# Optimization experiments

Measured on AMD Instinct MI355X. Metric: run time of the kernel, lower is better.

The kernel has to match this reference:

```python
import jax, jax.numpy as jnp
import numpy as np

T, D, H, E, V, WN = 4096, 128, 512, 256, 50000, 4


def setup_inputs() -> dict:
    key = jax.random.key(0)
    ks = jax.random.split(key, 16)
    x = jax.random.normal(ks[0], (T, D), jnp.float32)
    word_ids = jax.random.randint(ks[1], (T, WN), 0, V, dtype=jnp.int32)
    lens = jax.random.randint(ks[2], (T, WN), 2, 7)  # word lengths in [2,6]
    starts = jnp.arange(T)[:, None] - lens + 1       # word ending at t starts at t-len+1
    valid = starts >= 0
    word_mask = jnp.logical_and(valid, jax.random.uniform(ks[3], (T, WN)) < 0.3)
    word_starts = jnp.maximum(starts, 0).astype(jnp.int32)
    h0 = jax.random.normal(ks[4], (H,), jnp.float32)
    c0 = jax.random.normal(ks[5], (H,), jnp.float32)
    emb = jax.random.normal(ks[6], (V, E), jnp.float32)
    s_d, s_h, s_e = 1.0 / np.sqrt(D), 1.0 / np.sqrt(H), 1.0 / np.sqrt(E)
    W = jax.random.normal(ks[7], (D, 3 * H), jnp.float32) * s_d
    U = jax.random.normal(ks[8], (H, 3 * H), jnp.float32) * s_h
    b = jnp.zeros((3 * H,), jnp.float32)
    Wa = jax.random.normal(ks[9], (D, H), jnp.float32) * s_d
    Ua = jax.random.normal(ks[10], (H, H), jnp.float32) * s_h
    ba = jnp.zeros((H,), jnp.float32)
    Ww = jax.random.normal(ks[11], (E, 3 * H), jnp.float32) * s_e
    Uw = jax.random.normal(ks[12], (H, 3 * H), jnp.float32) * s_h
    bw = jnp.zeros((3 * H,), jnp.float32)
    return {"x": x, "word_ids": word_ids, "word_starts": word_starts,
            "word_mask": word_mask, "h0": h0, "c0": c0, "emb": emb,
            "W": W, "U": U, "b": b, "Wa": Wa, "Ua": Ua, "ba": ba,
            "Ww": Ww, "Uw": Uw, "bw": bw}


def _lattice_forward(x, word_ids, word_starts, word_mask, h0, c0, emb,
                     W, U, b, Wa, Ua, ba, Ww, Uw, bw):
    Tn = x.shape[0]
    Hn = h0.shape[0]

    def step(carry, inp):
        h_prev, c_prev, Hbuf, Cbuf, t = carry
        xt, wids, wstarts, wmask = inp
        # --- WordLSTMCell for lexicon words ending at t (started at wstarts) ---
        h_s = Hbuf[wstarts]                     # [WN, H] post-step states at starts
        c_s = Cbuf[wstarts]                     # [WN, H]
        x_w = emb[wids]                         # [WN, E] (word_dropout in eval mode)
        gw = x_w @ Ww + h_s @ Uw + bw           # [WN, 3H]
        f_w, i_w, g_w = jnp.split(gw, 3, axis=-1)
        c_w = jax.nn.sigmoid(f_w) * c_s + jax.nn.sigmoid(i_w) * jnp.tanh(g_w)
        # --- MultiInputLSTMCell at position t ---
        gates = xt @ W + h_prev @ U + b         # [3H]
        i_g, o_g, g_g = jnp.split(gates, 3)
        i_g = jax.nn.sigmoid(i_g)
        o_g = jax.nn.sigmoid(o_g)
        g_g = jnp.tanh(g_g)
        alpha = jax.nn.sigmoid(xt @ Wa + ba + c_w @ Ua)   # [WN, H]
        e = jnp.exp(jnp.concatenate([i_g[None, :], alpha], axis=0))  # [1+WN, H]
        m = jnp.concatenate([jnp.ones((1,), bool), wmask])
        e = e * m[:, None]
        wts = e / jnp.sum(e, axis=0)
        cand = jnp.concatenate([g_g[None, :], c_w], axis=0)
        c_soft = jnp.sum(wts * cand, axis=0)
        c_plain = (1.0 - i_g) * c_prev + i_g * g_g        # candidate_num == 0 branch
        c1 = jnp.where(jnp.any(wmask), c_soft, c_plain)
        h1 = o_g * jnp.tanh(c1)
        Hbuf = Hbuf.at[t].set(h1)
        Cbuf = Cbuf.at[t].set(c1)
        return (h1, c1, Hbuf, Cbuf, t + 1), (h1, c1)

    carry0 = (h0, c0, jnp.zeros((Tn, Hn), x.dtype), jnp.zeros((Tn, Hn), x.dtype),
              jnp.int32(0))
    _, (hs, cs) = jax.lax.scan(step, carry0, (x, word_ids, word_starts, word_mask))
    return jnp.concatenate([hs, cs], axis=-1)   # [T, 2H] hidden|cell states


def reference(x, word_ids, word_starts, word_mask, h0, c0, emb,
              W, U, b, Wa, Ua, ba, Ww, Uw, bw):
    return _lattice_forward(x, word_ids, word_starts, word_mask, h0, c0, emb,
                            W, U, b, Wa, Ua, ba, Ww, Uw, bw)
```

## Files before the change

### kernel.cpp

```cpp
#include <hip/hip_runtime.h>
#include <hip/hip_bf16.h>

typedef __hip_bfloat16 bf16;
typedef _Float16 half2v __attribute__((ext_vector_type(2)));

#define T_LEN 4096
#define D_IN  128
#define H_DIM 512
#define E_DIM 256
#define WNUM  4
#define G3    1536
#define NBLK  64

#define OFF_MODE   0ull
#define OFF_FMODE  4ull
#define OFF_HPK    16384ull
#define OFF_CWPK   (OFF_HPK + 8ull*512ull*4ull)
#define OFF_A      65536ull
#define OFF_AXA    (OFF_A   + 4096ull*1536ull*2ull)
#define OFF_GW0    (OFF_AXA + 4096ull*512ull*2ull)

__device__ __forceinline__ float bf2f(bf16 h) {
  unsigned short u = __builtin_bit_cast(unsigned short, h);
  unsigned int i = ((unsigned int)u) << 16;
  return __builtin_bit_cast(float, i);
}
__device__ __forceinline__ unsigned short f2bfbits(float f) {
  return __builtin_bit_cast(unsigned short, __float2bfloat16(f));
}
__device__ __forceinline__ unsigned int packbf(float a, float b) {
  return (unsigned int)f2bfbits(a) | ((unsigned int)f2bfbits(b) << 16);
}
__device__ __forceinline__ float sigm(float x) { return 1.f / (1.f + __expf(-x)); }
__device__ __forceinline__ float tanhfast(float x) { return 1.f - 2.f / (__expf(2.f * x) + 1.f); }

#if __has_builtin(__builtin_amdgcn_fdot2)
__device__ __forceinline__ float fdot2(half2v a, half2v b, float c) {
  return __builtin_amdgcn_fdot2(a, b, c, false);
}
#else
__device__ __forceinline__ float fdot2(half2v a, half2v b, float c) {
  return c + (float)a.x * (float)b.x + (float)a.y * (float)b.y;
}
#endif

__device__ __forceinline__ half2v make2(float a, float b) {
  half2v r; r.x = (_Float16)a; r.y = (_Float16)b; return r;
}

__device__ __forceinline__ unsigned int pack16(float v, int tag) {
  _Float16 h = (_Float16)v;
  unsigned short b = __builtin_bit_cast(unsigned short, h);
  return ((unsigned int)tag << 16) | (unsigned int)b;
}
__device__ __forceinline__ _Float16 unpack16(unsigned int v) {
  return __builtin_bit_cast(_Float16, (unsigned short)(v & 0xffffu));
}
__device__ __forceinline__ unsigned int aload(const unsigned int* p) {
  return __hip_atomic_load(p, __ATOMIC_RELAXED, __HIP_MEMORY_SCOPE_AGENT);
}
__device__ __forceinline__ void astore(unsigned int* p, unsigned int v) {
  __hip_atomic_store(p, v, __ATOMIC_RELAXED, __HIP_MEMORY_SCOPE_AGENT);
}

__device__ __forceinline__ float ldf(const void* p, size_t i, int fm) {
  return fm ? ((const float*)p)[i] : bf2f(((const bf16*)p)[i]);
}
__device__ __forceinline__ void ld8(const void* p, size_t i, int fm, float* o) {
  if (fm) {
    const float* q = (const float*)p + i;
    float4 a = *(const float4*)q, b2 = *(const float4*)(q + 4);
    o[0]=a.x; o[1]=a.y; o[2]=a.z; o[3]=a.w; o[4]=b2.x; o[5]=b2.y; o[6]=b2.z; o[7]=b2.w;
  } else {
    uint4 raw = *(const uint4*)((const bf16*)p + i);
    unsigned int u[4] = {raw.x, raw.y, raw.z, raw.w};
#pragma unroll
    for (int j = 0; j < 4; ++j) {
      o[2*j]   = __builtin_bit_cast(float, u[j] << 16);
      o[2*j+1] = __builtin_bit_cast(float, u[j] & 0xffff0000u);
    }
  }
}
__device__ __forceinline__ void ld4(const void* p, size_t i, int fm, float* o) {
  if (fm) {
    float4 a = *(const float4*)((const float*)p + i);
    o[0]=a.x; o[1]=a.y; o[2]=a.z; o[3]=a.w;
  } else {
    uint2 raw = *(const uint2*)((const bf16*)p + i);
    o[0] = __builtin_bit_cast(float, raw.x << 16);
    o[1] = __builtin_bit_cast(float, raw.x & 0xffff0000u);
    o[2] = __builtin_bit_cast(float, raw.y << 16);
    o[3] = __builtin_bit_cast(float, raw.y & 0xffff0000u);
  }
}
__device__ __forceinline__ bool readmask(const void* p, int idx, int mode) {
  switch (mode) {
    case 0:  return ((const int*)p)[idx] != 0;
    case 1:  return ((const unsigned char*)p)[idx] != 0;
    case 2:  return ((const unsigned short*)p)[idx] != 0;
    default: return ((const unsigned int*)p)[idx] != 0;
  }
}

__global__ void k_init(const void* __restrict__ mask_p, const void* __restrict__ h0_p,
                       unsigned char* __restrict__ ws) {
  int tid = threadIdx.x;
  __shared__ int s_b1, s_bf, s_f32, s_votes;
  if (tid == 0) { s_b1 = 0; s_bf = 0; s_f32 = 0; s_votes = 0; }
  __syncthreads();
  int b1 = 0, bfh = 0, f32h = 0;
  const unsigned int* dv = (const unsigned int*)mask_p;
  for (int i = tid; i < 4096; i += 256) {
    unsigned int d = dv[i];
    if (((d >> 8) & 0xFFu) == 1u || ((d >> 16) & 0xFFu) == 1u || ((d >> 24) & 0xFFu) == 1u) b1 = 1;
    if ((d & 0xFFFFu) == 0x3F80u) bfh = 1;
    if (d == 0x3F800000u) f32h = 1;
  }
  if (b1)  atomicOr(&s_b1, 1);
  if (bfh) atomicOr(&s_bf, 1);
  if (f32h) atomicOr(&s_f32, 1);
  if (tid < 128) {
    unsigned int d = ((const unsigned int*)h0_p)[tid];
    int e = (int)((d >> 23) & 0xFF);
    if (e >= 100 && e <= 140) atomicAdd(&s_votes, 1);
  }
  __syncthreads();
  if (tid == 0) {
    int mode = s_b1 ? 1 : (s_bf ? 2 : (s_f32 ? 3 : 0));
    *(int*)(ws + OFF_MODE)  = mode;
    *(int*)(ws + OFF_FMODE) = (s_votes >= 64) ? 1 : 0;
  }
}

__global__ __launch_bounds__(256) void k_xgemm(
    const void* __restrict__ x, const void* __restrict__ W, const void* __restrict__ b,
    const void* __restrict__ Wa, const void* __restrict__ ba, unsigned char* __restrict__ ws) {
  const int fm = *(const int*)(ws + OFF_FMODE);
  bf16* A   = (bf16*)(ws + OFF_A);
  bf16* Axa = (bf16*)(ws + OFF_AXA);
  const int tid = threadIdx.x;
  const int t0 = blockIdx.x * 8;
  __shared__ float sx[8][128];
  {
    int flat = tid * 4, r = flat >> 7, k = flat & 127;
    ld4(x, (size_t)(t0 + r) * D_IN + k, fm, &sx[r][k]);
  }
  __syncthreads();
  const bool isA = (tid < 192);
  const int c0 = isA ? tid * 8 : (tid - 192) * 8;
  const void* M = isA ? W : Wa;
  const int ldm = isA ? G3 : H_DIM;
  float acc[8][8];
#pragma unroll
  for (int r = 0; r < 8; ++r)
#pragma unroll
    for (int c = 0; c < 8; ++c) acc[r][c] = 0.f;
  for (int k = 0; k < D_IN; ++k) {
    float wv[8];
    ld8(M, (size_t)k * ldm + c0, fm, wv);
#pragma unroll
    for (int r = 0; r < 8; ++r) {
      float xv = sx[r][k];
#pragma unroll
      for (int c = 0; c < 8; ++c) acc[r][c] += xv * wv[c];
    }
  }
  float bias[8];
  ld8(isA ? b : ba, c0, fm, bias);
#pragma unroll
  for (int r = 0; r < 8; ++r) {
    uint4 o;
    o.x = packbf(acc[r][0] + bias[0], acc[r][1] + bias[1]);
    o.y = packbf(acc[r][2] + bias[2], acc[r][3] + bias[3]);
    o.z = packbf(acc[r][4] + bias[4], acc[r][5] + bias[5]);
    o.w = packbf(acc[r][6] + bias[6], acc[r][7] + bias[7]);
    if (isA) *(uint4*)(A + (size_t)(t0 + r) * G3 + c0) = o;
    else     *(uint4*)(Axa + (size_t)(t0 + r) * H_DIM + c0) = o;
  }
}

__global__ __launch_bounds__(256) void k_wgemm(
    const int* __restrict__ wids, const void* __restrict__ wmask,
    const void* __restrict__ emb, const void* __restrict__ Ww, const void* __restrict__ bw,
    unsigned char* __restrict__ ws) {
  const int mode = *(const int*)(ws + OFF_MODE);
  const int fm   = *(const int*)(ws + OFF_FMODE);
  bf16* GW0 = (bf16*)(ws + OFF_GW0);
  const int tid = threadIdx.x;
  const int r0 = blockIdx.x * 8;
  bool m[8]; bool any = false;
#pragma unroll
  for (int r = 0; r < 8; ++r) {
    bool mm = readmask(wmask, r0 + r, mode);
    m[r] = mm; any |= mm;
  }
  if (!any) return;
  __shared__ float se[8][E_DIM];
#pragma unroll
  for (int r = 0; r < 8; ++r)
    if (m[r]) {
      int wid = wids[r0 + r];
      se[r][tid] = ldf(emb, (size_t)wid * E_DIM + tid, fm);
    }
  __syncthreads();
  if (tid < 192) {
    const int c0 = tid * 8;
    float acc[8][8];
#pragma unroll
    for (int r = 0; r < 8; ++r)
#pragma unroll
      for (int c = 0; c < 8; ++c) acc[r][c] = 0.f;
    for (int k = 0; k < E_DIM; ++k) {
      float wv[8];
      ld8(Ww, (size_t)k * G3 + c0, fm, wv);
#pragma unroll
      for (int r = 0; r < 8; ++r)
        if (m[r]) {
          float xv = se[r][k];
#pragma unroll
          for (int c = 0; c < 8; ++c) acc[r][c] += xv * wv[c];
        }
    }
    float bias[8];
    ld8(bw, c0, fm, bias);
#pragma unroll
    for (int r = 0; r < 8; ++r)
      if (m[r]) {
        uint4 o;
        o.x = packbf(acc[r][0] + bias[0], acc[r][1] + bias[1]);
        o.y = packbf(acc[r][2] + bias[2], acc[r][3] + bias[3]);
        o.z = packbf(acc[r][4] + bias[4], acc[r][5] + bias[5]);
        o.w = packbf(acc[r][6] + bias[6], acc[r][7] + bias[7]);
        *(uint4*)(GW0 + (size_t)(r0 + r) * G3 + c0) = o;
      }
  }
}

#define PASS(slotptr, wt, accvar) do {                                  \
    float _acc = 0.f;                                                   \
    const _Float16* _vp = (slotptr) + 8 * rg;                           \
    _Pragma("unroll")                                                   \
    for (int _m = 0; _m < 8; ++_m) {                                    \
      float4 _raw = *(const float4*)(_vp + 64 * _m);                    \
      half2v _h0 = __builtin_bit_cast(half2v, _raw.x);                  \
      half2v _h1 = __builtin_bit_cast(half2v, _raw.y);                  \
      half2v _h2 = __builtin_bit_cast(half2v, _raw.z);                  \
      half2v _h3 = __builtin_bit_cast(half2v, _raw.w);                  \
      _acc = fdot2(_h0, wt[_m * 4 + 0], _acc);                          \
      _acc = fdot2(_h1, wt[_m * 4 + 1], _acc);                          \
      _acc = fdot2(_h2, wt[_m * 4 + 2], _acc);                          \
      _acc = fdot2(_h3, wt[_m * 4 + 3], _acc);                          \
    }                                                                   \
    accvar = _acc;                                                      \
  } while (0)

__global__ __launch_bounds__(256, 1) void k_seq(
    const int* __restrict__ wstarts, const void* __restrict__ wmask,
    const void* __restrict__ h0_p, const void* __restrict__ c0_p,
    const void* __restrict__ U, const void* __restrict__ Uw, const void* __restrict__ Ua,
    unsigned char* __restrict__ ws, void* __restrict__ outp) {
  const int tid = threadIdx.x;
  const int blk = blockIdx.x;
  const int wv = tid >> 6;
  const int lane = tid & 63;
  const int cg = lane >> 3;
  const int rg = lane & 7;
  const int kbase = blk * 8 + wv * 2;

  const int mode = *(const int*)(ws + OFF_MODE);
  const int fm   = *(const int*)(ws + OFF_FMODE);
  const bf16* A   = (const bf16*)(ws + OFF_A);
  const bf16* Axa = (const bf16*)(ws + OFF_AXA);
  const bf16* GW0 = (const bf16*)(ws + OFF_GW0);
  unsigned int* HPK  = (unsigned int*)(ws + OFF_HPK);
  unsigned int* CWPK = (unsigned int*)(ws + OFF_CWPK);

  __shared__ __align__(16) _Float16 hring[8][520];
  __shared__ __align__(16) _Float16 cwlds[WNUM][520];
  __shared__ float cring[8][8];
  __shared__ float scr[4][8];
  __shared__ float cwown[4][WNUM][2];

  {
    _Float16* hz = &hring[0][0];
    for (int i = tid; i < 8 * 520; i += 256) hz[i] = (_Float16)0.f;
    _Float16* cz = &cwlds[0][0];
    for (int i = tid; i < WNUM * 520; i += 256) cz[i] = (_Float16)0.f;
    if (tid < 64) (&cring[0][0])[tid] = 0.f;
    if (tid < 32) (&scr[0][0])[tid] = 0.f;
    if (tid < 32) (&cwown[0][0][0])[tid] = 0.f;
  }

  half2v wU[32], wUw[32], wUa[32];
  {
    const int gate = cg >> 1;
    const int klw = cg & 1;
    const int colU = gate * H_DIM + (kbase + klw);
    const int colA = kbase + cg;
#pragma unroll
    for (int mq = 0; mq < 32; ++mq) {
      int mm = mq >> 2, q = mq & 3;
      int r = 64 * mm + 8 * rg + 2 * q;
      float u0 = 0, u1 = 0, v0 = 0, v1 = 0, a0 = 0, a1 = 0;
      if (cg < 6) {
        u0 = ldf(U, (size_t)r * G3 + colU, fm);  u1 = ldf(U, (size_t)(r + 1) * G3 + colU, fm);
        v0 = ldf(Uw, (size_t)r * G3 + colU, fm); v1 = ldf(Uw, (size_t)(r + 1) * G3 + colU, fm);
      }
      if (cg < 2) {
        a0 = ldf(Ua, (size_t)r * H_DIM + colA, fm); a1 = ldf(Ua, (size_t)(r + 1) * H_DIM + colA, fm);
      }
      wU[mq] = make2(u0, u1); wUw[mq] = make2(v0, v1); wUa[mq] = make2(a0, a1);
    }
  }
  __syncthreads();

  {
    int i = tid * 2;
    hring[7][i]     = (_Float16)ldf(h0_p, i, fm);
    hring[7][i + 1] = (_Float16)ldf(h0_p, i + 1, fm);
    if (tid < 8) cring[7][tid] = ldf(c0_p, blk * 8 + tid, fm);
  }
  __syncthreads();

  for (int t = 0; t < T_LEN; ++t) {
    int st[WNUM]; bool val[WNUM]; bool anyw = false;
    float gwx[WNUM][6], aT[6], axaT[2];
#pragma unroll
    for (int w = 0; w < WNUM; ++w) {
      st[w] = wstarts[t * WNUM + w];
      bool mmk = readmask(wmask, t * WNUM + w, mode);
      val[w] = mmk; anyw |= mmk;
    }
#pragma unroll
    for (int w = 0; w < WNUM; ++w) {
#pragma unroll
      for (int g3 = 0; g3 < 3; ++g3) {
        unsigned int u = *(const unsigned int*)(GW0 + (size_t)(t * WNUM + w) * G3 + g3 * H_DIM + kbase);
        gwx[w][g3 * 2]     = __builtin_bit_cast(float, u << 16);
        gwx[w][g3 * 2 + 1] = __builtin_bit_cast(float, u & 0xffff0000u);
      }
    }
#pragma unroll
    for (int g3 = 0; g3 < 3; ++g3) {
      unsigned int u = *(const unsigned int*)(A + (size_t)t * G3 + g3 * H_DIM + kbase);
      aT[g3 * 2]     = __builtin_bit_cast(float, u << 16);
      aT[g3 * 2 + 1] = __builtin_bit_cast(float, u & 0xffff0000u);
    }
    {
      unsigned int u = *(const unsigned int*)(Axa + (size_t)t * H_DIM + kbase);
      axaT[0] = __builtin_bit_cast(float, u << 16);
      axaT[1] = __builtin_bit_cast(float, u & 0xffff0000u);
    }

    unsigned int* cwSlot = CWPK + (size_t)(t & 1) * WNUM * H_DIM;
#pragma unroll
    for (int w = 0; w < WNUM; ++w)
      if (val[w] && st[w] <= t - 2) {
        float accw;
        PASS(&hring[st[w] & 7][0], wUw, accw);
        float red = accw;
        red += __shfl_xor(red, 1); red += __shfl_xor(red, 2); red += __shfl_xor(red, 4);
        if (rg == 0 && cg < 6) scr[wv][cg] = red;
#pragma unroll
        for (int kl = 0; kl < 2; ++kl) {
          float f_ = scr[wv][0 + kl] + gwx[w][0 + kl];
          float i_ = scr[wv][2 + kl] + gwx[w][2 + kl];
          float g_ = scr[wv][4 + kl] + gwx[w][4 + kl];
          float cs = cring[st[w] & 7][wv * 2 + kl];
          float cw = sigm(f_) * cs + sigm(i_) * tanhfast(g_);
          if (lane == 0) {
            cwown[wv][w][kl] = cw;
            astore(cwSlot + w * H_DIM + kbase + kl, pack16(cw, t + 1));
          }
        }
      }

    if (t > 0) {
      const unsigned int expect = (unsigned int)t;
      const unsigned int* hp = HPK + (size_t)((t - 1) & 7) * H_DIM + tid * 2;
      unsigned int v0 = aload(hp);
      unsigned int v1 = aload(hp + 1);
      while ((v0 >> 16) != expect || (v1 >> 16) != expect) {
        __builtin_amdgcn_s_sleep(2);
        v0 = aload(hp);
        v1 = aload(hp + 1);
      }
      int sl = (t - 1) & 7;
      hring[sl][tid * 2]     = unpack16(v0);
      hring[sl][tid * 2 + 1] = unpack16(v1);
    }
    __syncthreads();

#pragma unroll
    for (int w = 0; w < WNUM; ++w)
      if (val[w] && st[w] > t - 2) {
        float accw;
        PASS(&hring[(t - 1) & 7][0], wUw, accw);
        float red = accw;
        red += __shfl_xor(red, 1); red += __shfl_xor(red, 2); red += __shfl_xor(red, 4);
        if (rg == 0 && cg < 6) scr[wv][cg] = red;
#pragma unroll
        for (int kl = 0; kl < 2; ++kl) {
          float f_ = scr[wv][0 + kl] + gwx[w][0 + kl];
          float i_ = scr[wv][2 + kl] + gwx[w][2 + kl];
          float g_ = scr[wv][4 + kl] + gwx[w][4 + kl];
          float cs = cring[st[w] & 7][wv * 2 + kl];
          float cw = sigm(f_) * cs + sigm(i_) * tanhfast(g_);
          if (lane == 0) {
            cwown[wv][w][kl] = cw;
            astore(cwSlot + w * H_DIM + kbase + kl, pack16(cw, t + 1));
          }
        }
      }

    float ig[2], og[2], gg[2];
    {
      float accu;
      PASS(&hring[(t - 1) & 7][0], wU, accu);
      float red = accu;
      red += __shfl_xor(red, 1); red += __shfl_xor(red, 2); red += __shfl_xor(red, 4);
      if (rg == 0 && cg < 6) scr[wv][cg] = red;
#pragma unroll
      for (int kl = 0; kl < 2; ++kl) {
        ig[kl] = sigm(scr[wv][0 + kl] + aT[0 + kl]);
        og[kl] = sigm(scr[wv][2 + kl] + aT[2 + kl]);
        gg[kl] = tanhfast(scr[wv][4 + kl] + aT[4 + kl]);
      }
    }

#pragma unroll
    for (int w = 0; w < WNUM; ++w)
      if (val[w]) {
        const unsigned int expect = (unsigned int)(t + 1);
        const unsigned int* cp = cwSlot + w * H_DIM + tid * 2;
        unsigned int v0 = aload(cp);
        unsigned int v1 = aload(cp + 1);
        while ((v0 >> 16) != expect || (v1 >> 16) != expect) {
          __builtin_amdgcn_s_sleep(2);
          v0 = aload(cp);
          v1 = aload(cp + 1);
        }
        cwlds[w][tid * 2]     = unpack16(v0);
        cwlds[w][tid * 2 + 1] = unpack16(v1);
      }
    __syncthreads();

    float aw[WNUM][2] = {{0.f,0.f},{0.f,0.f},{0.f,0.f},{0.f,0.f}};
#pragma unroll
    for (int w = 0; w < WNUM; ++w)
      if (val[w]) {
        float acca;
        PASS(&cwlds[w][0], wUa, acca);
        float red = acca;
        red += __shfl_xor(red, 1); red += __shfl_xor(red, 2); red += __shfl_xor(red, 4);
        if (rg == 0 && cg < 2) scr[wv][cg] = red;
        aw[w][0] = scr[wv][0]; aw[w][1] = scr[wv][1];
      }

#pragma unroll
    for (int kl = 0; kl < 2; ++kl) {
      int kg = kbase + kl;
      float e0 = __expf(ig[kl]);
      float num = e0 * gg[kl], den = e0;
#pragma unroll
      for (int w = 0; w < WNUM; ++w)
        if (val[w]) {
          float al = sigm(aw[w][kl] + axaT[kl]);
          float ew = __expf(al);
          num += ew * cwown[wv][w][kl];
          den += ew;
        }
      float cprev = cring[(t - 1) & 7][wv * 2 + kl];
      float csoft = num / den;
      float cplain = (1.f - ig[kl]) * cprev + ig[kl] * gg[kl];
      float c1 = anyw ? csoft : cplain;
      float h1 = og[kl] * tanhfast(c1);
      if (lane == kl) {
        cring[t & 7][wv * 2 + kl] = c1;
        astore(HPK + (size_t)(t & 7) * H_DIM + kg, pack16(h1, t + 1));
        if (fm) {
          ((float*)outp)[(size_t)t * 1024 + kg] = h1;
          ((float*)outp)[(size_t)t * 1024 + 512 + kg] = c1;
        } else {
          ((bf16*)outp)[(size_t)t * 1024 + kg] = __float2bfloat16(h1);
          ((bf16*)outp)[(size_t)t * 1024 + 512 + kg] = __float2bfloat16(c1);
        }
      }
    }
  }
}

extern "C" void kernel_launch(void* const* d_in, const int* in_sizes, int n_in,
                              void* d_out, int out_size, void* d_ws, size_t ws_size,
                              hipStream_t stream) {
  const void* x    = d_in[0];
  const int* wids  = (const int*)d_in[1];
  const int* wst   = (const int*)d_in[2];
  const void* wmsk = d_in[3];
  const void* h0   = d_in[4];
  const void* c0   = d_in[5];
  const void* emb  = d_in[6];
  const void* W    = d_in[7];
  const void* U    = d_in[8];
  const void* b    = d_in[9];
  const void* Wa   = d_in[10];
  const void* Ua   = d_in[11];
  const void* ba   = d_in[12];
  const void* Ww   = d_in[13];
  const void* Uw   = d_in[14];
  const void* bw   = d_in[15];
  unsigned char* ws = (unsigned char*)d_ws;
  (void)in_sizes; (void)n_in; (void)out_size; (void)ws_size;

  k_init<<<1, 256, 0, stream>>>(wmsk, h0, ws);
  k_xgemm<<<512, 256, 0, stream>>>(x, W, b, Wa, ba, ws);
  k_wgemm<<<2048, 256, 0, stream>>>(wids, wmsk, emb, Ww, bw, ws);
  k_seq<<<NBLK, 256, 0, stream>>>(wst, wmsk, h0, c0, U, Uw, Ua, ws, d_out);
}
```

Before: 17.81 ms.

## Software-pipeline next-step inputs and early word-cell work across timesteps

Restructures the sequential recurrence loop so that the per-step inputs (word starts, masks, GW0/A/Axa projections) for step t+1 are prefetched during step t. Word cells whose start state is already available are computed at the end of the previous step rather than at the top of the current one. Their results are then polled from the packed exchange buffer together with the late word cells. The aim is to take global-load latency and early word-LSTM matvecs off the critical path between the h-exchange barriers. In exchange it adds register pressure and an extra barrier at the top of each step.

```diff
diff --git a/kernel.cpp b/kernel.cpp
--- a/kernel.cpp
+++ b/kernel.cpp
@@ -254,6 +254,21 @@
     accvar = _acc;                                                      \
   } while (0)
 
+#define CW_BODY(gwxARR, stARR, w, slotptr, tagv) do {                   \
+    _Pragma("unroll")                                                   \
+    for (int kl = 0; kl < 2; ++kl) {                                    \
+      float f_ = scr[wv][0 + kl] + gwxARR[w][0 + kl];                   \
+      float i_ = scr[wv][2 + kl] + gwxARR[w][2 + kl];                   \
+      float g_ = scr[wv][4 + kl] + gwxARR[w][4 + kl];                   \
+      float cs = cring[stARR[w] & 7][wv * 2 + kl];                      \
+      float cw = sigm(f_) * cs + sigm(i_) * tanhfast(g_);               \
+      if (lane == 0) {                                                  \
+        cwown[wv][w][kl] = cw;                                          \
+        astore((slotptr) + w * H_DIM + kbase + kl, pack16(cw, (tagv))); \
+      }                                                                 \
+    }                                                                   \
+  } while (0)
+
 __global__ __launch_bounds__(256, 1) void k_seq(
     const int* __restrict__ wstarts, const void* __restrict__ wmask,
     const void* __restrict__ h0_p, const void* __restrict__ c0_p,
@@ -322,58 +337,87 @@
   }
   __syncthreads();
 
+  int stC[WNUM]; bool valC[WNUM]; bool anyC = false;
+#pragma unroll
+  for (int w = 0; w < WNUM; ++w) {
+    stC[w] = wstarts[w];
+    valC[w] = readmask(wmask, w, mode);
+    anyC |= valC[w];
+  }
+  float gwxC[WNUM][6], aTC[6], axaC[2];
+#pragma unroll
+  for (int w = 0; w < WNUM; ++w)
+#pragma unroll
+    for (int j = 0; j < 6; ++j) gwxC[w][j] = 0.f;
+#pragma unroll
+  for (int w = 0; w < WNUM; ++w)
+    if (valC[w]) {
+#pragma unroll
+      for (int g3 = 0; g3 < 3; ++g3) {
+        unsigned int u = *(const unsigned int*)(GW0 + (size_t)w * G3 + g3 * H_DIM + kbase);
+        gwxC[w][g3 * 2]     = __builtin_bit_cast(float, u << 16);
+        gwxC[w][g3 * 2 + 1] = __builtin_bit_cast(float, u & 0xffff0000u);
+      }
+    }
+#pragma unroll
+  for (int g3 = 0; g3 < 3; ++g3) {
+    unsigned int u = *(const unsigned int*)(A + (size_t)g3 * H_DIM + kbase);
+    aTC[g3 * 2]     = __builtin_bit_cast(float, u << 16);
+    aTC[g3 * 2 + 1] = __builtin_bit_cast(float, u & 0xffff0000u);
+  }
+  {
+    unsigned int u = *(const unsigned int*)(Axa + kbase);
+    axaC[0] = __builtin_bit_cast(float, u << 16);
+    axaC[1] = __builtin_bit_cast(float, u & 0xffff0000u);
+  }
+
   for (int t = 0; t < T_LEN; ++t) {
-    int st[WNUM]; bool val[WNUM]; bool anyw = false;
-    float gwx[WNUM][6], aT[6], axaT[2];
+    __syncthreads();
+
+    const int tn = t + 1;
+    const bool haveN = (tn < T_LEN);
+    const int tm = haveN ? tn : t;
+    int stN[WNUM]; bool valN[WNUM]; bool anyN = false;
 #pragma unroll
     for (int w = 0; w < WNUM; ++w) {
-      st[w] = wstarts[t * WNUM + w];
-      bool mmk = readmask(wmask, t * WNUM + w, mode);
-      val[w] = mmk; anyw |= mmk;
-    }
-#pragma unroll
-    for (int w = 0; w < WNUM; ++w) {
-#pragma unroll
-      for (int g3 = 0; g3 < 3; ++g3) {
-        unsigned int u = *(const unsigned int*)(GW0 + (size_t)(t * WNUM + w) * G3 + g3 * H_DIM + kbase);
-        gwx[w][g3 * 2]     = __builtin_bit_cast(float, u << 16);
-        gwx[w][g3 * 2 + 1] = __builtin_bit_cast(float, u & 0xffff0000u);
-      }
-    }
-#pragma unroll
-    for (int g3 = 0; g3 < 3; ++g3) {
-      unsigned int u = *(const unsigned int*)(A + (size_t)t * G3 + g3 * H_DIM + kbase);
-      aT[g3 * 2]     = __builtin_bit_cast(float, u << 16);
-      aT[g3 * 2 + 1] = __builtin_bit_cast(float, u & 0xffff0000u);
-    }
+      stN[w] = wstarts[tm * WNUM + w];
+      bool v = haveN && readmask(wmask, tm * WNUM + w, mode);
+      valN[w] = v; anyN |= v;
+    }
+
+    unsigned int* cwSlotC = CWPK + (size_t)(t & 1) * WNUM * H_DIM;
+
     {
-      unsigned int u = *(const unsigned int*)(Axa + (size_t)t * H_DIM + kbase);
-      axaT[0] = __builtin_bit_cast(float, u << 16);
-      axaT[1] = __builtin_bit_cast(float, u & 0xffff0000u);
-    }
-
-    unsigned int* cwSlot = CWPK + (size_t)(t & 1) * WNUM * H_DIM;
-#pragma unroll
-    for (int w = 0; w < WNUM; ++w)
-      if (val[w] && st[w] <= t - 2) {
-        float accw;
-        PASS(&hring[st[w] & 7][0], wUw, accw);
-        float red = accw;
-        red += __shfl_xor(red, 1); red += __shfl_xor(red, 2); red += __shfl_xor(red, 4);
-        if (rg == 0 && cg < 6) scr[wv][cg] = red;
-#pragma unroll
-        for (int kl = 0; kl < 2; ++kl) {
-          float f_ = scr[wv][0 + kl] + gwx[w][0 + kl];
-          float i_ = scr[wv][2 + kl] + gwx[w][2 + kl];
-          float g_ = scr[wv][4 + kl] + gwx[w][4 + kl];
-          float cs = cring[st[w] & 7][wv * 2 + kl];
-          float cw = sigm(f_) * cs + sigm(i_) * tanhfast(g_);
-          if (lane == 0) {
-            cwown[wv][w][kl] = cw;
-            astore(cwSlot + w * H_DIM + kbase + kl, pack16(cw, t + 1));
+      bool need[WNUM];
+      bool pending = false;
+#pragma unroll
+      for (int w = 0; w < WNUM; ++w) {
+        need[w] = valC[w] && stC[w] <= t - 2;
+        pending |= need[w];
+      }
+      const unsigned int expect = (unsigned int)(t + 1);
+      while (pending) {
+        unsigned int got[WNUM][2];
+#pragma unroll
+        for (int w = 0; w < WNUM; ++w)
+          if (need[w]) {
+            const unsigned int* cp = cwSlotC + w * H_DIM + tid * 2;
+            got[w][0] = aload(cp); got[w][1] = aload(cp + 1);
           }
-        }
-      }
+        bool still = false;
+#pragma unroll
+        for (int w = 0; w < WNUM; ++w)
+          if (need[w]) {
+            if ((got[w][0] >> 16) == expect && (got[w][1] >> 16) == expect) {
+              cwlds[w][tid * 2]     = unpack16(got[w][0]);
+              cwlds[w][tid * 2 + 1] = unpack16(got[w][1]);
+              need[w] = false;
+            } else still = true;
+          }
+        pending = still;
+        if (pending) __builtin_amdgcn_s_sleep(2);
+      }
+    }
 
     if (t > 0) {
       const unsigned int expect = (unsigned int)t;
@@ -391,26 +435,17 @@
     }
     __syncthreads();
 
+    bool anyLate = false;
 #pragma unroll
     for (int w = 0; w < WNUM; ++w)
-      if (val[w] && st[w] > t - 2) {
+      if (valC[w] && stC[w] > t - 2) {
+        anyLate = true;
         float accw;
         PASS(&hring[(t - 1) & 7][0], wUw, accw);
         float red = accw;
         red += __shfl_xor(red, 1); red += __shfl_xor(red, 2); red += __shfl_xor(red, 4);
         if (rg == 0 && cg < 6) scr[wv][cg] = red;
-#pragma unroll
-        for (int kl = 0; kl < 2; ++kl) {
-          float f_ = scr[wv][0 + kl] + gwx[w][0 + kl];
-          float i_ = scr[wv][2 + kl] + gwx[w][2 + kl];
-          float g_ = scr[wv][4 + kl] + gwx[w][4 + kl];
-          float cs = cring[st[w] & 7][wv * 2 + kl];
-          float cw = sigm(f_) * cs + sigm(i_) * tanhfast(g_);
-          if (lane == 0) {
-            cwown[wv][w][kl] = cw;
-            astore(cwSlot + w * H_DIM + kbase + kl, pack16(cw, t + 1));
-          }
-        }
+        CW_BODY(gwxC, stC, w, cwSlotC, t + 1);
       }
 
     float ig[2], og[2], gg[2];
@@ -422,33 +457,79 @@
       if (rg == 0 && cg < 6) scr[wv][cg] = red;
 #pragma unroll
       for (int kl = 0; kl < 2; ++kl) {
-        ig[kl] = sigm(scr[wv][0 + kl] + aT[0 + kl]);
-        og[kl] = sigm(scr[wv][2 + kl] + aT[2 + kl]);
-        gg[kl] = tanhfast(scr[wv][4 + kl] + aT[4 + kl]);
-      }
-    }
-
+        ig[kl] = sigm(scr[wv][0 + kl] + aTC[0 + kl]);
+        og[kl] = sigm(scr[wv][2 + kl] + aTC[2 + kl]);
+        gg[kl] = tanhfast(scr[wv][4 + kl] + aTC[4 + kl]);
+      }
+    }
+
+    float gwxN[WNUM][6], aTN[6], axaN[2];
 #pragma unroll
     for (int w = 0; w < WNUM; ++w)
-      if (val[w]) {
-        const unsigned int expect = (unsigned int)(t + 1);
-        const unsigned int* cp = cwSlot + w * H_DIM + tid * 2;
-        unsigned int v0 = aload(cp);
-        unsigned int v1 = aload(cp + 1);
-        while ((v0 >> 16) != expect || (v1 >> 16) != expect) {
-          __builtin_amdgcn_s_sleep(2);
-          v0 = aload(cp);
-          v1 = aload(cp + 1);
+#pragma unroll
+      for (int j = 0; j < 6; ++j) gwxN[w][j] = 0.f;
+    aTN[0]=aTN[1]=aTN[2]=aTN[3]=aTN[4]=aTN[5]=0.f; axaN[0]=axaN[1]=0.f;
+    if (haveN) {
+#pragma unroll
+      for (int w = 0; w < WNUM; ++w)
+        if (valN[w]) {
+#pragma unroll
+          for (int g3 = 0; g3 < 3; ++g3) {
+            unsigned int u = *(const unsigned int*)(GW0 + (size_t)(tn * WNUM + w) * G3 + g3 * H_DIM + kbase);
+            gwxN[w][g3 * 2]     = __builtin_bit_cast(float, u << 16);
+            gwxN[w][g3 * 2 + 1] = __builtin_bit_cast(float, u & 0xffff0000u);
+          }
         }
-        cwlds[w][tid * 2]     = unpack16(v0);
-        cwlds[w][tid * 2 + 1] = unpack16(v1);
-      }
+#pragma unroll
+      for (int g3 = 0; g3 < 3; ++g3) {
+        unsigned int u = *(const unsigned int*)(A + (size_t)tn * G3 + g3 * H_DIM + kbase);
+        aTN[g3 * 2]     = __builtin_bit_cast(float, u << 16);
+        aTN[g3 * 2 + 1] = __builtin_bit_cast(float, u & 0xffff0000u);
+      }
+      {
+        unsigned int u = *(const unsigned int*)(Axa + (size_t)tn * H_DIM + kbase);
+        axaN[0] = __builtin_bit_cast(float, u << 16);
+        axaN[1] = __builtin_bit_cast(float, u & 0xffff0000u);
+      }
+    }
+
+    if (anyLate) {
+      bool need[WNUM];
+      bool pending = false;
+#pragma unroll
+      for (int w = 0; w < WNUM; ++w) {
+        need[w] = valC[w] && stC[w] > t - 2;
+        pending |= need[w];
+      }
+      const unsigned int expect = (unsigned int)(t + 1);
+      while (pending) {
+        unsigned int got[WNUM][2];
+#pragma unroll
+        for (int w = 0; w < WNUM; ++w)
+          if (need[w]) {
+            const unsigned int* cp = cwSlotC + w * H_DIM + tid * 2;
+            got[w][0] = aload(cp); got[w][1] = aload(cp + 1);
+          }
+        bool still = false;
+#pragma unroll
+        for (int w = 0; w < WNUM; ++w)
+          if (need[w]) {
+            if ((got[w][0] >> 16) == expect && (got[w][1] >> 16) == expect) {
+              cwlds[w][tid * 2]     = unpack16(got[w][0]);
+              cwlds[w][tid * 2 + 1] = unpack16(got[w][1]);
+              need[w] = false;
+            } else still = true;
+          }
+        pending = still;
+        if (pending) __builtin_amdgcn_s_sleep(2);
+      }
+    }
     __syncthreads();
 
     float aw[WNUM][2] = {{0.f,0.f},{0.f,0.f},{0.f,0.f},{0.f,0.f}};
 #pragma unroll
     for (int w = 0; w < WNUM; ++w)
-      if (val[w]) {
+      if (valC[w]) {
         float acca;
         PASS(&cwlds[w][0], wUa, acca);
         float red = acca;
@@ -457,15 +538,15 @@
         aw[w][0] = scr[wv][0]; aw[w][1] = scr[wv][1];
       }
 
+    float c1v[2], h1v[2];
 #pragma unroll
     for (int kl = 0; kl < 2; ++kl) {
-      int kg = kbase + kl;
       float e0 = __expf(ig[kl]);
       float num = e0 * gg[kl], den = e0;
 #pragma unroll
       for (int w = 0; w < WNUM; ++w)
-        if (val[w]) {
-          float al = sigm(aw[w][kl] + axaT[kl]);
+        if (valC[w]) {
+          float al = sigm(aw[w][kl] + axaC[kl]);
           float ew = __expf(al);
           num += ew * cwown[wv][w][kl];
           den += ew;
@@ -473,20 +554,50 @@
       float cprev = cring[(t - 1) & 7][wv * 2 + kl];
       float csoft = num / den;
       float cplain = (1.f - ig[kl]) * cprev + ig[kl] * gg[kl];
-      float c1 = anyw ? csoft : cplain;
-      float h1 = og[kl] * tanhfast(c1);
+      c1v[kl] = anyC ? csoft : cplain;
+      h1v[kl] = og[kl] * tanhfast(c1v[kl]);
       if (lane == kl) {
-        cring[t & 7][wv * 2 + kl] = c1;
-        astore(HPK + (size_t)(t & 7) * H_DIM + kg, pack16(h1, t + 1));
+        cring[t & 7][wv * 2 + kl] = c1v[kl];
+        astore(HPK + (size_t)(t & 7) * H_DIM + kbase + kl, pack16(h1v[kl], t + 1));
+      }
+    }
+#pragma unroll
+    for (int kl = 0; kl < 2; ++kl)
+      if (lane == kl) {
+        int kg = kbase + kl;
         if (fm) {
-          ((float*)outp)[(size_t)t * 1024 + kg] = h1;
-          ((float*)outp)[(size_t)t * 1024 + 512 + kg] = c1;
+          ((float*)outp)[(size_t)t * 1024 + kg] = h1v[kl];
+          ((float*)outp)[(size_t)t * 1024 + 512 + kg] = c1v[kl];
         } else {
-          ((bf16*)outp)[(size_t)t * 1024 + kg] = __float2bfloat16(h1);
-          ((bf16*)outp)[(size_t)t * 1024 + 512 + kg] = __float2bfloat16(c1);
+          ((bf16*)outp)[(size_t)t * 1024 + kg] = __float2bfloat16(h1v[kl]);
+          ((bf16*)outp)[(size_t)t * 1024 + 512 + kg] = __float2bfloat16(c1v[kl]);
         }
       }
-    }
+
+    if (haveN) {
+      unsigned int* cwSlotN = CWPK + (size_t)(tn & 1) * WNUM * H_DIM;
+#pragma unroll
+      for (int w = 0; w < WNUM; ++w)
+        if (valN[w] && stN[w] <= t - 1) {
+          float accw;
+          PASS(&hring[stN[w] & 7][0], wUw, accw);
+          float red = accw;
+          red += __shfl_xor(red, 1); red += __shfl_xor(red, 2); red += __shfl_xor(red, 4);
+          if (rg == 0 && cg < 6) scr[wv][cg] = red;
+          CW_BODY(gwxN, stN, w, cwSlotN, t + 2);
+        }
+    }
+
+    anyC = anyN;
+#pragma unroll
+    for (int w = 0; w < WNUM; ++w) {
+      stC[w] = stN[w]; valC[w] = valN[w];
+#pragma unroll
+      for (int j = 0; j < 6; ++j) gwxC[w][j] = gwxN[w][j];
+    }
+#pragma unroll
+    for (int j = 0; j < 6; ++j) aTC[j] = aTN[j];
+    axaC[0] = axaN[0]; axaC[1] = axaN[1];
   }
 }
 
```

Measured after the change: 20.57 ms. +15.5%, slower.

## Shrink recurrent kernel to 16 blocks with 8 columns per wave and flag sync

Applied to the files above, without the earlier changes.

The persistent sequential kernel now runs on 16 blocks instead of 64. Each wave owns 8 hidden columns across all three gates and keeps three gate weight slices in registers, so all 64 lanes do useful dot-product work where several lane groups used to idle. Per-wave progress flags are added for the hidden-state and word-cell exchanges: waves poll a 64-entry flag array with a wave-wide vote before reading packed values, which is meant to cut cross-block polling traffic and the number of participants in each step's global exchange. The cost is three times more register-resident weights per thread and more serial work per wave per step.

```diff
diff --git a/kernel.cpp b/kernel.cpp
--- a/kernel.cpp
+++ b/kernel.cpp
@@ -10,10 +10,12 @@
 #define E_DIM 256
 #define WNUM  4
 #define G3    1536
-#define NBLK  64
+#define NBLK  16
 
 #define OFF_MODE   0ull
 #define OFF_FMODE  4ull
+#define OFF_HFLG   1024ull
+#define OFF_CWFLG  2048ull
 #define OFF_HPK    16384ull
 #define OFF_CWPK   (OFF_HPK + 8ull*512ull*4ull)
 #define OFF_A      65536ull
@@ -124,6 +126,10 @@
     int e = (int)((d >> 23) & 0xFF);
     if (e >= 100 && e <= 140) atomicAdd(&s_votes, 1);
   }
+  if (tid < 64) {
+    ((unsigned int*)(ws + OFF_HFLG))[tid] = 0u;
+    ((unsigned int*)(ws + OFF_CWFLG))[tid] = 0u;
+  }
   __syncthreads();
   if (tid == 0) {
     int mode = s_b1 ? 1 : (s_bf ? 2 : (s_f32 ? 3 : 0));
@@ -156,13 +162,13 @@
 #pragma unroll
     for (int c = 0; c < 8; ++c) acc[r][c] = 0.f;
   for (int k = 0; k < D_IN; ++k) {
-    float wv[8];
-    ld8(M, (size_t)k * ldm + c0, fm, wv);
+    float wvv[8];
+    ld8(M, (size_t)k * ldm + c0, fm, wvv);
 #pragma unroll
     for (int r = 0; r < 8; ++r) {
       float xv = sx[r][k];
 #pragma unroll
-      for (int c = 0; c < 8; ++c) acc[r][c] += xv * wv[c];
+      for (int c = 0; c < 8; ++c) acc[r][c] += xv * wvv[c];
     }
   }
   float bias[8];
@@ -211,14 +217,14 @@
 #pragma unroll
       for (int c = 0; c < 8; ++c) acc[r][c] = 0.f;
     for (int k = 0; k < E_DIM; ++k) {
-      float wv[8];
-      ld8(Ww, (size_t)k * G3 + c0, fm, wv);
+      float wvv[8];
+      ld8(Ww, (size_t)k * G3 + c0, fm, wvv);
 #pragma unroll
       for (int r = 0; r < 8; ++r)
         if (m[r]) {
           float xv = se[r][k];
 #pragma unroll
-          for (int c = 0; c < 8; ++c) acc[r][c] += xv * wv[c];
+          for (int c = 0; c < 8; ++c) acc[r][c] += xv * wvv[c];
         }
     }
     float bias[8];
@@ -236,8 +242,8 @@
   }
 }
 
-#define PASS(slotptr, wt, accvar) do {                                  \
-    float _acc = 0.f;                                                   \
+#define PASS3(slotptr, wt0, wt1, wt2) do {                              \
+    float _a0 = 0.f, _a1 = 0.f, _a2 = 0.f;                              \
     const _Float16* _vp = (slotptr) + 8 * rg;                           \
     _Pragma("unroll")                                                   \
     for (int _m = 0; _m < 8; ++_m) {                                    \
@@ -246,12 +252,34 @@
       half2v _h1 = __builtin_bit_cast(half2v, _raw.y);                  \
       half2v _h2 = __builtin_bit_cast(half2v, _raw.z);                  \
       half2v _h3 = __builtin_bit_cast(half2v, _raw.w);                  \
-      _acc = fdot2(_h0, wt[_m * 4 + 0], _acc);                          \
-      _acc = fdot2(_h1, wt[_m * 4 + 1], _acc);                          \
-      _acc = fdot2(_h2, wt[_m * 4 + 2], _acc);                          \
-      _acc = fdot2(_h3, wt[_m * 4 + 3], _acc);                          \
+      _a0 = fdot2(_h0, wt0[_m*4+0], _a0); _a0 = fdot2(_h1, wt0[_m*4+1], _a0); \
+      _a0 = fdot2(_h2, wt0[_m*4+2], _a0); _a0 = fdot2(_h3, wt0[_m*4+3], _a0); \
+      _a1 = fdot2(_h0, wt1[_m*4+0], _a1); _a1 = fdot2(_h1, wt1[_m*4+1], _a1); \
+      _a1 = fdot2(_h2, wt1[_m*4+2], _a1); _a1 = fdot2(_h3, wt1[_m*4+3], _a1); \
+      _a2 = fdot2(_h0, wt2[_m*4+0], _a2); _a2 = fdot2(_h1, wt2[_m*4+1], _a2); \
+      _a2 = fdot2(_h2, wt2[_m*4+2], _a2); _a2 = fdot2(_h3, wt2[_m*4+3], _a2); \
     }                                                                   \
-    accvar = _acc;                                                      \
+    _a0 += __shfl_xor(_a0,1); _a0 += __shfl_xor(_a0,2); _a0 += __shfl_xor(_a0,4); \
+    _a1 += __shfl_xor(_a1,1); _a1 += __shfl_xor(_a1,2); _a1 += __shfl_xor(_a1,4); \
+    _a2 += __shfl_xor(_a2,1); _a2 += __shfl_xor(_a2,2); _a2 += __shfl_xor(_a2,4); \
+    if (rg == 0) { scr[wv][cg] = _a0; scr[wv][8+cg] = _a1; scr[wv][16+cg] = _a2; } \
+  } while (0)
+
+#define PASS1(slotptr, wt) do {                                         \
+    float _a = 0.f;                                                     \
+    const _Float16* _vp = (slotptr) + 8 * rg;                           \
+    _Pragma("unroll")                                                   \
+    for (int _m = 0; _m < 8; ++_m) {                                    \
+      float4 _raw = *(const float4*)(_vp + 64 * _m);                    \
+      half2v _h0 = __builtin_bit_cast(half2v, _raw.x);                  \
+      half2v _h1 = __builtin_bit_cast(half2v, _raw.y);                  \
+      half2v _h2 = __builtin_bit_cast(half2v, _raw.z);                  \
+      half2v _h3 = __builtin_bit_cast(half2v, _raw.w);                  \
+      _a = fdot2(_h0, wt[_m*4+0], _a); _a = fdot2(_h1, wt[_m*4+1], _a); \
+      _a = fdot2(_h2, wt[_m*4+2], _a); _a = fdot2(_h3, wt[_m*4+3], _a); \
+    }                                                                   \
+    _a += __shfl_xor(_a,1); _a += __shfl_xor(_a,2); _a += __shfl_xor(_a,4); \
+    if (rg == 0) scr[wv][24+cg] = _a;                                   \
   } while (0)
 
 __global__ __launch_bounds__(256, 1) void k_seq(
@@ -265,51 +293,51 @@
   const int lane = tid & 63;
   const int cg = lane >> 3;
   const int rg = lane & 7;
-  const int kbase = blk * 8 + wv * 2;
+  const int kbase = blk * 32 + wv * 8;
+  const int fidx = blk * 4 + wv;
 
   const int mode = *(const int*)(ws + OFF_MODE);
   const int fm   = *(const int*)(ws + OFF_FMODE);
   const bf16* A   = (const bf16*)(ws + OFF_A);
   const bf16* Axa = (const bf16*)(ws + OFF_AXA);
   const bf16* GW0 = (const bf16*)(ws + OFF_GW0);
-  unsigned int* HPK  = (unsigned int*)(ws + OFF_HPK);
-  unsigned int* CWPK = (unsigned int*)(ws + OFF_CWPK);
+  unsigned int* HPK   = (unsigned int*)(ws + OFF_HPK);
+  unsigned int* CWPK  = (unsigned int*)(ws + OFF_CWPK);
+  unsigned int* HFLG  = (unsigned int*)(ws + OFF_HFLG);
+  unsigned int* CWFLG = (unsigned int*)(ws + OFF_CWFLG);
 
   __shared__ __align__(16) _Float16 hring[8][520];
   __shared__ __align__(16) _Float16 cwlds[WNUM][520];
-  __shared__ float cring[8][8];
-  __shared__ float scr[4][8];
-  __shared__ float cwown[4][WNUM][2];
+  __shared__ float scr[4][32];
+  __shared__ float cring[4][8][8];
 
   {
     _Float16* hz = &hring[0][0];
     for (int i = tid; i < 8 * 520; i += 256) hz[i] = (_Float16)0.f;
     _Float16* cz = &cwlds[0][0];
     for (int i = tid; i < WNUM * 520; i += 256) cz[i] = (_Float16)0.f;
-    if (tid < 64) (&cring[0][0])[tid] = 0.f;
-    if (tid < 32) (&scr[0][0])[tid] = 0.f;
-    if (tid < 32) (&cwown[0][0][0])[tid] = 0.f;
-  }
-
-  half2v wU[32], wUw[32], wUa[32];
+    if (tid < 128) (&scr[0][0])[tid] = 0.f;
+    float* cr = &cring[0][0][0];
+    for (int i = tid; i < 256; i += 256) cr[i] = 0.f;
+  }
+
+  half2v wU[3][32], wUw[3][32], wUa[32];
+#pragma unroll
+  for (int g = 0; g < 3; ++g) {
+    const int colU = g * H_DIM + kbase + cg;
+#pragma unroll
+    for (int mq = 0; mq < 32; ++mq) {
+      int r = 64 * (mq >> 2) + 8 * rg + 2 * (mq & 3);
+      wU[g][mq]  = make2(ldf(U,  (size_t)r * G3 + colU, fm), ldf(U,  (size_t)(r + 1) * G3 + colU, fm));
+      wUw[g][mq] = make2(ldf(Uw, (size_t)r * G3 + colU, fm), ldf(Uw, (size_t)(r + 1) * G3 + colU, fm));
+    }
+  }
   {
-    const int gate = cg >> 1;
-    const int klw = cg & 1;
-    const int colU = gate * H_DIM + (kbase + klw);
     const int colA = kbase + cg;
 #pragma unroll
     for (int mq = 0; mq < 32; ++mq) {
-      int mm = mq >> 2, q = mq & 3;
-      int r = 64 * mm + 8 * rg + 2 * q;
-      float u0 = 0, u1 = 0, v0 = 0, v1 = 0, a0 = 0, a1 = 0;
-      if (cg < 6) {
-        u0 = ldf(U, (size_t)r * G3 + colU, fm);  u1 = ldf(U, (size_t)(r + 1) * G3 + colU, fm);
-        v0 = ldf(Uw, (size_t)r * G3 + colU, fm); v1 = ldf(Uw, (size_t)(r + 1) * G3 + colU, fm);
-      }
-      if (cg < 2) {
-        a0 = ldf(Ua, (size_t)r * H_DIM + colA, fm); a1 = ldf(Ua, (size_t)(r + 1) * H_DIM + colA, fm);
-      }
-      wU[mq] = make2(u0, u1); wUw[mq] = make2(v0, v1); wUa[mq] = make2(a0, a1);
+      int r = 64 * (mq >> 2) + 8 * rg + 2 * (mq & 3);
+      wUa[mq] = make2(ldf(Ua, (size_t)r * H_DIM + colA, fm), ldf(Ua, (size_t)(r + 1) * H_DIM + colA, fm));
     }
   }
   __syncthreads();
@@ -318,72 +346,65 @@
     int i = tid * 2;
     hring[7][i]     = (_Float16)ldf(h0_p, i, fm);
     hring[7][i + 1] = (_Float16)ldf(h0_p, i + 1, fm);
-    if (tid < 8) cring[7][tid] = ldf(c0_p, blk * 8 + tid, fm);
+    if (lane < 8) cring[wv][7][lane] = ldf(c0_p, kbase + lane, fm);
   }
   __syncthreads();
 
   for (int t = 0; t < T_LEN; ++t) {
     int st[WNUM]; bool val[WNUM]; bool anyw = false;
-    float gwx[WNUM][6], aT[6], axaT[2];
 #pragma unroll
     for (int w = 0; w < WNUM; ++w) {
       st[w] = wstarts[t * WNUM + w];
       bool mmk = readmask(wmask, t * WNUM + w, mode);
       val[w] = mmk; anyw |= mmk;
     }
-#pragma unroll
-    for (int w = 0; w < WNUM; ++w) {
-#pragma unroll
-      for (int g3 = 0; g3 < 3; ++g3) {
-        unsigned int u = *(const unsigned int*)(GW0 + (size_t)(t * WNUM + w) * G3 + g3 * H_DIM + kbase);
-        gwx[w][g3 * 2]     = __builtin_bit_cast(float, u << 16);
-        gwx[w][g3 * 2 + 1] = __builtin_bit_cast(float, u & 0xffff0000u);
-      }
-    }
-#pragma unroll
-    for (int g3 = 0; g3 < 3; ++g3) {
-      unsigned int u = *(const unsigned int*)(A + (size_t)t * G3 + g3 * H_DIM + kbase);
-      aT[g3 * 2]     = __builtin_bit_cast(float, u << 16);
-      aT[g3 * 2 + 1] = __builtin_bit_cast(float, u & 0xffff0000u);
-    }
-    {
-      unsigned int u = *(const unsigned int*)(Axa + (size_t)t * H_DIM + kbase);
-      axaT[0] = __builtin_bit_cast(float, u << 16);
-      axaT[1] = __builtin_bit_cast(float, u & 0xffff0000u);
+    float aT0 = 0.f, aT1 = 0.f, aT2 = 0.f, axa = 0.f;
+    float gw[WNUM][3];
+#pragma unroll
+    for (int w = 0; w < WNUM; ++w) { gw[w][0] = 0.f; gw[w][1] = 0.f; gw[w][2] = 0.f; }
+    if (lane < 8) {
+      const int col = kbase + lane;
+      aT0 = bf2f(A[(size_t)t * G3 + col]);
+      aT1 = bf2f(A[(size_t)t * G3 + H_DIM + col]);
+      aT2 = bf2f(A[(size_t)t * G3 + 2 * H_DIM + col]);
+      axa = bf2f(Axa[(size_t)t * H_DIM + col]);
+#pragma unroll
+      for (int w = 0; w < WNUM; ++w) {
+#pragma unroll
+        for (int g = 0; g < 3; ++g)
+          gw[w][g] = bf2f(GW0[(size_t)(t * WNUM + w) * G3 + g * H_DIM + col]);
+      }
     }
 
     unsigned int* cwSlot = CWPK + (size_t)(t & 1) * WNUM * H_DIM;
+    float cwown[WNUM] = {0.f, 0.f, 0.f, 0.f};
+
 #pragma unroll
     for (int w = 0; w < WNUM; ++w)
       if (val[w] && st[w] <= t - 2) {
-        float accw;
-        PASS(&hring[st[w] & 7][0], wUw, accw);
-        float red = accw;
-        red += __shfl_xor(red, 1); red += __shfl_xor(red, 2); red += __shfl_xor(red, 4);
-        if (rg == 0 && cg < 6) scr[wv][cg] = red;
-#pragma unroll
-        for (int kl = 0; kl < 2; ++kl) {
-          float f_ = scr[wv][0 + kl] + gwx[w][0 + kl];
-          float i_ = scr[wv][2 + kl] + gwx[w][2 + kl];
-          float g_ = scr[wv][4 + kl] + gwx[w][4 + kl];
-          float cs = cring[st[w] & 7][wv * 2 + kl];
+        PASS3(&hring[st[w] & 7][0], wUw[0], wUw[1], wUw[2]);
+        if (lane < 8) {
+          float f_ = scr[wv][lane]      + gw[w][0];
+          float i_ = scr[wv][8 + lane]  + gw[w][1];
+          float g_ = scr[wv][16 + lane] + gw[w][2];
+          float cs = cring[wv][st[w] & 7][lane];
           float cw = sigm(f_) * cs + sigm(i_) * tanhfast(g_);
-          if (lane == 0) {
-            cwown[wv][w][kl] = cw;
-            astore(cwSlot + w * H_DIM + kbase + kl, pack16(cw, t + 1));
-          }
+          cwown[w] = cw;
+          astore(cwSlot + w * H_DIM + kbase + lane, pack16(cw, t + 1));
         }
       }
 
     if (t > 0) {
-      const unsigned int expect = (unsigned int)t;
+      unsigned int f = aload(HFLG + lane);
+      while (!__all((int)(f >= (unsigned int)t))) {
+        __builtin_amdgcn_s_sleep(1);
+        f = aload(HFLG + lane);
+      }
       const unsigned int* hp = HPK + (size_t)((t - 1) & 7) * H_DIM + tid * 2;
-      unsigned int v0 = aload(hp);
-      unsigned int v1 = aload(hp + 1);
-      while ((v0 >> 16) != expect || (v1 >> 16) != expect) {
-        __builtin_amdgcn_s_sleep(2);
-        v0 = aload(hp);
-        v1 = aload(hp + 1);
+      unsigned int v0 = aload(hp), v1 = aload(hp + 1);
+      while ((v0 >> 16) != (unsigned int)t || (v1 >> 16) != (unsigned int)t) {
+        __builtin_amdgcn_s_sleep(1);
+        v0 = aload(hp); v1 = aload(hp + 1);
       }
       int sl = (t - 1) & 7;
       hring[sl][tid * 2]     = unpack16(v0);
@@ -394,99 +415,84 @@
 #pragma unroll
     for (int w = 0; w < WNUM; ++w)
       if (val[w] && st[w] > t - 2) {
-        float accw;
-        PASS(&hring[(t - 1) & 7][0], wUw, accw);
-        float red = accw;
-        red += __shfl_xor(red, 1); red += __shfl_xor(red, 2); red += __shfl_xor(red, 4);
-        if (rg == 0 && cg < 6) scr[wv][cg] = red;
-#pragma unroll
-        for (int kl = 0; kl < 2; ++kl) {
-          float f_ = scr[wv][0 + kl] + gwx[w][0 + kl];
-          float i_ = scr[wv][2 + kl] + gwx[w][2 + kl];
-          float g_ = scr[wv][4 + kl] + gwx[w][4 + kl];
-          float cs = cring[st[w] & 7][wv * 2 + kl];
+        PASS3(&hring[(t - 1) & 7][0], wUw[0], wUw[1], wUw[2]);
+        if (lane < 8) {
+          float f_ = scr[wv][lane]      + gw[w][0];
+          float i_ = scr[wv][8 + lane]  + gw[w][1];
+          float g_ = scr[wv][16 + lane] + gw[w][2];
+          float cs = cring[wv][st[w] & 7][lane];
           float cw = sigm(f_) * cs + sigm(i_) * tanhfast(g_);
-          if (lane == 0) {
-            cwown[wv][w][kl] = cw;
-            astore(cwSlot + w * H_DIM + kbase + kl, pack16(cw, t + 1));
+          cwown[w] = cw;
+          astore(cwSlot + w * H_DIM + kbase + lane, pack16(cw, t + 1));
+        }
+      }
+    if (lane == 0) astore(CWFLG + fidx, (unsigned int)(t + 1));
+
+    float ig = 0.f, og = 0.f, gg = 0.f;
+    PASS3(&hring[(t - 1) & 7][0], wU[0], wU[1], wU[2]);
+    if (lane < 8) {
+      ig = sigm(scr[wv][lane] + aT0);
+      og = sigm(scr[wv][8 + lane] + aT1);
+      gg = tanhfast(scr[wv][16 + lane] + aT2);
+    }
+
+    if (anyw) {
+      unsigned int f = aload(CWFLG + lane);
+      while (!__all((int)(f >= (unsigned int)(t + 1)))) {
+        __builtin_amdgcn_s_sleep(1);
+        f = aload(CWFLG + lane);
+      }
+#pragma unroll
+      for (int w = 0; w < WNUM; ++w)
+        if (val[w]) {
+          const unsigned int* cp = cwSlot + w * H_DIM + tid * 2;
+          unsigned int v0 = aload(cp), v1 = aload(cp + 1);
+          while ((v0 >> 16) != (unsigned int)(t + 1) || (v1 >> 16) != (unsigned int)(t + 1)) {
+            __builtin_amdgcn_s_sleep(1);
+            v0 = aload(cp); v1 = aload(cp + 1);
           }
+          cwlds[w][tid * 2]     = unpack16(v0);
+          cwlds[w][tid * 2 + 1] = unpack16(v1);
         }
-      }
-
-    float ig[2], og[2], gg[2];
-    {
-      float accu;
-      PASS(&hring[(t - 1) & 7][0], wU, accu);
-      float red = accu;
-      red += __shfl_xor(red, 1); red += __shfl_xor(red, 2); red += __shfl_xor(red, 4);
-      if (rg == 0 && cg < 6) scr[wv][cg] = red;
-#pragma unroll
-      for (int kl = 0; kl < 2; ++kl) {
-        ig[kl] = sigm(scr[wv][0 + kl] + aT[0 + kl]);
-        og[kl] = sigm(scr[wv][2 + kl] + aT[2 + kl]);
-        gg[kl] = tanhfast(scr[wv][4 + kl] + aT[4 + kl]);
-      }
-    }
-
+      __syncthreads();
+    }
+
+    float aw[WNUM] = {0.f, 0.f, 0.f, 0.f};
 #pragma unroll
     for (int w = 0; w < WNUM; ++w)
       if (val[w]) {
-        const unsigned int expect = (unsigned int)(t + 1);
-        const unsigned int* cp = cwSlot + w * H_DIM + tid * 2;
-        unsigned int v0 = aload(cp);
-        unsigned int v1 = aload(cp + 1);
-        while ((v0 >> 16) != expect || (v1 >> 16) != expect) {
-          __builtin_amdgcn_s_sleep(2);
-          v0 = aload(cp);
-          v1 = aload(cp + 1);
-        }
-        cwlds[w][tid * 2]     = unpack16(v0);
-        cwlds[w][tid * 2 + 1] = unpack16(v1);
-      }
-    __syncthreads();
-
-    float aw[WNUM][2] = {{0.f,0.f},{0.f,0.f},{0.f,0.f},{0.f,0.f}};
-#pragma unroll
-    for (int w = 0; w < WNUM; ++w)
-      if (val[w]) {
-        float acca;
-        PASS(&cwlds[w][0], wUa, acca);
-        float red = acca;
-        red += __shfl_xor(red, 1); red += __shfl_xor(red, 2); red += __shfl_xor(red, 4);
-        if (rg == 0 && cg < 2) scr[wv][cg] = red;
-        aw[w][0] = scr[wv][0]; aw[w][1] = scr[wv][1];
-      }
-
-#pragma unroll
-    for (int kl = 0; kl < 2; ++kl) {
-      int kg = kbase + kl;
-      float e0 = __expf(ig[kl]);
-      float num = e0 * gg[kl], den = e0;
+        PASS1(&cwlds[w][0], wUa);
+        if (lane < 8) aw[w] = scr[wv][24 + lane];
+      }
+
+    if (lane < 8) {
+      float e0 = __expf(ig);
+      float num = e0 * gg, den = e0;
 #pragma unroll
       for (int w = 0; w < WNUM; ++w)
         if (val[w]) {
-          float al = sigm(aw[w][kl] + axaT[kl]);
+          float al = sigm(aw[w] + axa);
           float ew = __expf(al);
-          num += ew * cwown[wv][w][kl];
+          num += ew * cwown[w];
           den += ew;
         }
-      float cprev = cring[(t - 1) & 7][wv * 2 + kl];
+      float cprev = cring[wv][(t - 1) & 7][lane];
       float csoft = num / den;
-      float cplain = (1.f - ig[kl]) * cprev + ig[kl] * gg[kl];
+      float cplain = (1.f - ig) * cprev + ig * gg;
       float c1 = anyw ? csoft : cplain;
-      float h1 = og[kl] * tanhfast(c1);
-      if (lane == kl) {
-        cring[t & 7][wv * 2 + kl] = c1;
-        astore(HPK + (size_t)(t & 7) * H_DIM + kg, pack16(h1, t + 1));
-        if (fm) {
-          ((float*)outp)[(size_t)t * 1024 + kg] = h1;
-          ((float*)outp)[(size_t)t * 1024 + 512 + kg] = c1;
-        } else {
-          ((bf16*)outp)[(size_t)t * 1024 + kg] = __float2bfloat16(h1);
-          ((bf16*)outp)[(size_t)t * 1024 + 512 + kg] = __float2bfloat16(c1);
-        }
-      }
-    }
+      float h1 = og * tanhfast(c1);
+      cring[wv][t & 7][lane] = c1;
+      astore(HPK + (size_t)(t & 7) * H_DIM + kbase + lane, pack16(h1, t + 1));
+      const int kg = kbase + lane;
+      if (fm) {
+        ((float*)outp)[(size_t)t * 1024 + kg] = h1;
+        ((float*)outp)[(size_t)t * 1024 + 512 + kg] = c1;
+      } else {
+        ((bf16*)outp)[(size_t)t * 1024 + kg] = __float2bfloat16(h1);
+        ((bf16*)outp)[(size_t)t * 1024 + 512 + kg] = __float2bfloat16(c1);
+      }
+    }
+    if (lane == 0) astore(HFLG + fidx, (unsigned int)(t + 1));
   }
 }
 
```

Result: slower. 28.67 ms (+61.0%).
